# Kernel optimization log

Measured on AMD Instinct MI355X. Metric: run time of the kernel, lower is better.

Reference implementation:

```python
import jax, jax.numpy as jnp
import numpy as np

N_NODES = 100000
N_EDGES = 1600000
N_GRAPHS = 1000
F_IN, HID = 9, 64


def _glorot(key, shape):
    fan_in, fan_out = shape[0], shape[1]
    lim = (6.0 / (fan_in + fan_out)) ** 0.5
    return jax.random.uniform(key, shape, jnp.float32, -lim, lim)


def setup_inputs() -> dict:
    key = jax.random.key(0)
    ks = jax.random.split(key, 12)
    x = jax.random.normal(ks[0], (N_NODES, F_IN), jnp.float32)
    edge_index = jax.random.randint(ks[1], (2, N_EDGES), 0, N_NODES, jnp.int64)
    edge_attr = jnp.zeros((N_EDGES, 1), jnp.float32)
    batch = jnp.sort(jax.random.randint(ks[2], (N_NODES,), 0, N_GRAPHS, jnp.int64))
    # SAGEConv layer 1: 9 -> 64 (lin_l on aggregated neighbors w/ bias, lin_r on root)
    Wl1 = _glorot(ks[3], (F_IN, HID)); Wr1 = _glorot(ks[4], (F_IN, HID)); b1 = jnp.zeros((HID,), jnp.float32)
    # SAGEConv layer 2: 64 -> 64
    Wl2 = _glorot(ks[5], (HID, HID)); Wr2 = _glorot(ks[6], (HID, HID)); b2 = jnp.zeros((HID,), jnp.float32)
    # MLP readout: 64 -> 32 -> 1
    Wm1 = _glorot(ks[7], (HID, HID // 2)); bm1 = jnp.zeros((HID // 2,), jnp.float32)
    Wm2 = _glorot(ks[8], (HID // 2, 1)); bm2 = jnp.zeros((1,), jnp.float32)
    return dict(x=x, edge_index=edge_index, edge_attr=edge_attr, batch=batch,
                Wl1=Wl1, Wr1=Wr1, b1=b1, Wl2=Wl2, Wr2=Wr2, b2=b2,
                Wm1=Wm1, bm1=bm1, Wm2=Wm2, bm2=bm2)


def _sage_conv(x, src, dst, Wl, Wr, b, n_nodes):
    # mean aggregation of source-node features onto target nodes
    msgs = x[src]                                              # [E, F] gather
    s = jax.ops.segment_sum(msgs, dst, num_segments=n_nodes)   # [N, F] scatter-add
    cnt = jax.ops.segment_sum(jnp.ones((src.shape[0],), x.dtype), dst, num_segments=n_nodes)
    agg = s / jnp.maximum(cnt, 1.0)[:, None]
    return agg @ Wl + x @ Wr + b


def reference(x, edge_index, edge_attr, batch,
              Wl1, Wr1, b1, Wl2, Wr2, b2, Wm1, bm1, Wm2, bm2):
    src, dst = edge_index[0], edge_index[1]
    n = x.shape[0]
    h = jax.nn.relu(_sage_conv(x, src, dst, Wl1, Wr1, b1, n))
    h = _sage_conv(h, src, dst, Wl2, Wr2, b2, n)               # no act after last layer
    # global mean pool over graphs
    gs = jax.ops.segment_sum(h, batch, num_segments=N_GRAPHS)
    gc = jax.ops.segment_sum(jnp.ones((n,), h.dtype), batch, num_segments=N_GRAPHS)
    xg = gs / jnp.maximum(gc, 1.0)[:, None]                    # [G, 64]
    out = jax.nn.sigmoid(jax.nn.relu(xg @ Wm1 + bm1) @ Wm2 + bm2)  # [G, 1]
    return out
```

## Files before the change

kernel.cpp:

```cpp
#include <hip/hip_runtime.h>
#include <math.h>

#define N_NODES  100000
#define N_EDGES  1600000
#define N_GRAPHS 1000
#define F_IN     9
#define HID      64
#define NBUCK    196
#define BCAP     12288
#define CHUNK    4096
#define NZERO    128200
#define NPB      32

typedef unsigned int uint32;
typedef unsigned short ushort16;
typedef float v2f __attribute__((ext_vector_type(2)));


__device__ __forceinline__ uint32 pk_lo(float a, float b, uint32 old) {
    return (uint32)__builtin_amdgcn_cvt_pk_fp8_f32(a, b, (int)old, false);
}
__device__ __forceinline__ uint32 pk_hi(float a, float b, uint32 old) {
    return (uint32)__builtin_amdgcn_cvt_pk_fp8_f32(a, b, (int)old, true);
}
__device__ __forceinline__ float bfl(uint32 w) { return __uint_as_float(w << 16); }
__device__ __forceinline__ float bfh(uint32 w) { return __uint_as_float(w & 0xffff0000u); }
__device__ __forceinline__ uint32 f2bf1(float f) {
    uint32 u = __float_as_uint(f);
    u += 0x7fffu + ((u >> 16) & 1u);
    return u >> 16;
}
__device__ __forceinline__ uint32 bfpair(float lo, float hi) {
    return f2bf1(lo) | (f2bf1(hi) << 16);
}

__global__ __launch_bounds__(256) void zero_kernel(float4* __restrict__ ws) {
    int i = blockIdx.x * 256 + threadIdx.x;
    if (i * 4 < NZERO)
        ws[i] = make_float4(0.f, 0.f, 0.f, 0.f);
}

__global__ __launch_bounds__(256) void pad_part_kernel(const float* __restrict__ x,
                                                       const int* __restrict__ ei,
                                                       int* __restrict__ gcur,
                                                       int* __restrict__ ebuf,
                                                       uint32* __restrict__ x8b) {
    __shared__ int lcnt[NBUCK], lbase[NBUCK];
    int tid = threadIdx.x;

    int n = blockIdx.x * 256 + tid;
    if (n < N_NODES) {
        uint32 w[4];
        #pragma unroll
        for (int p = 0; p < 4; ++p) {
            float v0 = (4 * p + 0 < F_IN) ? x[(size_t)n * F_IN + 4 * p + 0] : 0.0f;
            float v1 = (4 * p + 1 < F_IN) ? x[(size_t)n * F_IN + 4 * p + 1] : 0.0f;
            float v2 = (4 * p + 2 < F_IN) ? x[(size_t)n * F_IN + 4 * p + 2] : 0.0f;
            float v3 = (4 * p + 3 < F_IN) ? x[(size_t)n * F_IN + 4 * p + 3] : 0.0f;
            w[p] = pk_hi(v2, v3, pk_lo(v0, v1, 0u));
        }
        *reinterpret_cast<uint4*>(&x8b[(size_t)n * 4]) =
            make_uint4(w[0], w[1], w[2], w[3]);
    }

    for (int i = tid; i < NBUCK; i += 256) lcnt[i] = 0;
    __syncthreads();
    int e0 = blockIdx.x * CHUNK;
    int e1 = e0 + CHUNK; if (e1 > N_EDGES) e1 = N_EDGES;
    for (int e = e0 + tid; e < e1; e += 256)
        atomicAdd(&lcnt[ei[N_EDGES + e] >> 9], 1);
    __syncthreads();
    for (int i = tid; i < NBUCK; i += 256)
        lbase[i] = atomicAdd(&gcur[i], lcnt[i]);
    __syncthreads();
    for (int i = tid; i < NBUCK; i += 256) lcnt[i] = 0;
    __syncthreads();
    for (int e = e0 + tid; e < e1; e += 256) {
        int src = ei[e];
        int dst = ei[N_EDGES + e];
        int b = dst >> 9;
        int pos = lbase[b] + atomicAdd(&lcnt[b], 1);
        if (pos < BCAP)
            ebuf[(size_t)b * BCAP + pos] = src | ((dst & 511) << 17);
    }
}

__global__ __launch_bounds__(512) void build_csr_kernel(const int* __restrict__ ebuf,
                                                        const int* __restrict__ gcur,
                                                        int2* __restrict__ rowcnt,
                                                        int* __restrict__ col) {
    __shared__ int cnt[512];
    __shared__ int cur[512];
    __shared__ int wsum[8];
    int b = blockIdx.x;
    int n0 = b << 9;
    int tid = threadIdx.x;
    int ec = gcur[b]; if (ec > BCAP) ec = BCAP;
    size_t base = (size_t)b * BCAP;
    cnt[tid] = 0;
    __syncthreads();
    for (int e = tid; e < ec; e += 512)
        atomicAdd(&cnt[(uint32)ebuf[base + e] >> 17], 1);
    __syncthreads();
    int v = cnt[tid];
    int lane = tid & 63, wid = tid >> 6;
    int s = v;
    #pragma unroll
    for (int off = 1; off < 64; off <<= 1) {
        int u = __shfl_up(s, off, 64);
        if (lane >= off) s += u;
    }
    if (lane == 63) wsum[wid] = s;
    __syncthreads();
    int add = 0;
    for (int w = 0; w < wid; ++w) add += wsum[w];
    int off_ex = s - v + add;
    int n = n0 + tid;
    if (n < N_NODES) rowcnt[n] = make_int2((int)base + off_ex, v);
    cur[tid] = off_ex;
    __syncthreads();
    for (int e = tid; e < ec; e += 512) {
        int pv = ebuf[base + e];
        int pos = atomicAdd(&cur[(uint32)pv >> 17], 1);
        col[base + pos] = pv & 0x1FFFF;
    }
}

__global__ __launch_bounds__(256) void agg_l1_kernel(const float* __restrict__ x,
                                                     const uint32* __restrict__ x8b,
                                                     const int2* __restrict__ rowcnt,
                                                     const int* __restrict__ col,
                                                     const float* __restrict__ Wl1,
                                                     const float* __restrict__ Wr1,
                                                     const float* __restrict__ b1,
                                                     const int* __restrict__ batch,
                                                     uint32* __restrict__ h1b,
                                                     float* __restrict__ poolH) {
    __shared__ float  w1s[F_IN * 128];
    __shared__ float  bs[HID];
    __shared__ float  ss[NPB * 20];
    __shared__ float  xs[NPB * 10];
    __shared__ uint32 hsp[NPB * 33];
    int tid = threadIdx.x;
    int n0 = blockIdx.x * NPB;
    for (int i = tid; i < F_IN * HID; i += 256) {
        int f = i >> 6, j = i & 63;
        w1s[f * 128 + j]      = Wl1[i];
        w1s[f * 128 + 64 + j] = Wr1[i];
    }
    if (tid < HID) bs[tid] = b1[tid];
    for (int i = tid; i < NPB * F_IN; i += 256) {
        int r = i / F_IN, f = i - r * F_IN;
        xs[r * 10 + f] = x[(size_t)(n0 + r) * F_IN + f];
    }

    {
        int r = tid >> 3, s = (tid >> 2) & 1, q = tid & 3;
        int2 rc = rowcnt[n0 + r];
        int deg = rc.y;
        v2f a01 = {0.f, 0.f}, a23 = {0.f, 0.f};
        int i = s;
        for (; i + 6 < deg; i += 8) {
            int c0 = col[rc.x + i];
            int c1 = col[rc.x + i + 2];
            int c2 = col[rc.x + i + 4];
            int c3 = col[rc.x + i + 6];
            uint32 d0 = x8b[(size_t)c0 * 4 + q];
            uint32 d1 = x8b[(size_t)c1 * 4 + q];
            uint32 d2 = x8b[(size_t)c2 * 4 + q];
            uint32 d3 = x8b[(size_t)c3 * 4 + q];
            a01 += __builtin_amdgcn_cvt_pk_f32_fp8((int)d0, false);
            a23 += __builtin_amdgcn_cvt_pk_f32_fp8((int)d0, true);
            a01 += __builtin_amdgcn_cvt_pk_f32_fp8((int)d1, false);
            a23 += __builtin_amdgcn_cvt_pk_f32_fp8((int)d1, true);
            a01 += __builtin_amdgcn_cvt_pk_f32_fp8((int)d2, false);
            a23 += __builtin_amdgcn_cvt_pk_f32_fp8((int)d2, true);
            a01 += __builtin_amdgcn_cvt_pk_f32_fp8((int)d3, false);
            a23 += __builtin_amdgcn_cvt_pk_f32_fp8((int)d3, true);
        }
        for (; i < deg; i += 2) {
            uint32 d0 = x8b[(size_t)col[rc.x + i] * 4 + q];
            a01 += __builtin_amdgcn_cvt_pk_f32_fp8((int)d0, false);
            a23 += __builtin_amdgcn_cvt_pk_f32_fp8((int)d0, true);
        }
        float r4[4] = {a01[0], a01[1], a23[0], a23[1]};
        #pragma unroll
        for (int k = 0; k < 4; ++k)
            r4[k] += __shfl_xor(r4[k], 4, 64);
        if (s == 0) {
            float inv = 1.0f / fmaxf((float)deg, 1.0f);
            *reinterpret_cast<float4*>(&ss[r * 20 + q * 4]) =
                make_float4(r4[0] * inv, r4[1] * inv, r4[2] * inv, r4[3] * inv);
        }
    }
    __syncthreads();

    int r = tid >> 3, cg = tid & 7, k0 = cg * 8;
    float h[8];
    #pragma unroll
    for (int kk = 0; kk < 8; ++kk) {
        int k = k0 + kk;
        float v = bs[k];
        #pragma unroll
        for (int f = 0; f < F_IN; ++f)
            v += ss[r * 20 + f] * w1s[f * 128 + k]
               + xs[r * 10 + f] * w1s[f * 128 + 64 + k];
        h[kk] = fmaxf(v, 0.0f);
    }
    int n = n0 + r;
    {
        uint32 w0 = pk_hi(h[2], h[3], pk_lo(h[0], h[1], 0u));
        uint32 w1 = pk_hi(h[6], h[7], pk_lo(h[4], h[5], 0u));
        *reinterpret_cast<uint2*>(&h1b[(size_t)n * 16 + cg * 2]) =
            make_uint2(w0, w1);
    }
    {
        hsp[r * 33 + cg * 4 + 0] = bfpair(h[0], h[1]);
        hsp[r * 33 + cg * 4 + 1] = bfpair(h[2], h[3]);
        hsp[r * 33 + cg * 4 + 2] = bfpair(h[4], h[5]);
        hsp[r * 33 + cg * 4 + 3] = bfpair(h[6], h[7]);
    }
    __syncthreads();
    if (tid < HID) {
        int j = tid;
        int wsel = j >> 1;
        bool hi = (j & 1) != 0;
        int cur = batch[n0];
        uint32 w0 = hsp[wsel];
        float v = hi ? bfh(w0) : bfl(w0);
        for (int rr = 1; rr < NPB; ++rr) {
            int g = batch[n0 + rr];
            uint32 wr = hsp[rr * 33 + wsel];
            float val = hi ? bfh(wr) : bfl(wr);
            if (g == cur) v += val;
            else { atomicAdd(&poolH[cur * HID + j], v); cur = g; v = val; }
        }
        atomicAdd(&poolH[cur * HID + j], v);
    }
}

__global__ __launch_bounds__(256) void gather2_kernel(const uint32* __restrict__ h1b,
                                                      const int2* __restrict__ rowcnt,
                                                      const int* __restrict__ col,
                                                      const int* __restrict__ batch,
                                                      float* __restrict__ poolA) {
    __shared__ float sh[4][HID];
    int w = threadIdx.x >> 6;
    int lane = threadIdx.x & 63;
    int slot = lane >> 3;
    int grp  = lane & 7;
    int n = blockIdx.x * 4 + w;
    int2 rc = rowcnt[n];
    const uint32* hb = h1b + grp * 2;
    v2f a0 = {0.f, 0.f}, a1 = {0.f, 0.f}, a2 = {0.f, 0.f}, a3 = {0.f, 0.f};
    int i = rc.x + slot;
    int end = rc.x + rc.y;
    for (; i + 8 < end; i += 16) {
        int c0 = col[i];
        int c1 = col[i + 8];
        uint2 d0 = *reinterpret_cast<const uint2*>(hb + (size_t)c0 * 16);
        uint2 d1 = *reinterpret_cast<const uint2*>(hb + (size_t)c1 * 16);
        a0 += __builtin_amdgcn_cvt_pk_f32_fp8((int)d0.x, false);
        a1 += __builtin_amdgcn_cvt_pk_f32_fp8((int)d0.x, true);
        a2 += __builtin_amdgcn_cvt_pk_f32_fp8((int)d0.y, false);
        a3 += __builtin_amdgcn_cvt_pk_f32_fp8((int)d0.y, true);
        a0 += __builtin_amdgcn_cvt_pk_f32_fp8((int)d1.x, false);
        a1 += __builtin_amdgcn_cvt_pk_f32_fp8((int)d1.x, true);
        a2 += __builtin_amdgcn_cvt_pk_f32_fp8((int)d1.y, false);
        a3 += __builtin_amdgcn_cvt_pk_f32_fp8((int)d1.y, true);
    }
    if (i < end) {
        int c0 = col[i];
        uint2 d0 = *reinterpret_cast<const uint2*>(hb + (size_t)c0 * 16);
        a0 += __builtin_amdgcn_cvt_pk_f32_fp8((int)d0.x, false);
        a1 += __builtin_amdgcn_cvt_pk_f32_fp8((int)d0.x, true);
        a2 += __builtin_amdgcn_cvt_pk_f32_fp8((int)d0.y, false);
        a3 += __builtin_amdgcn_cvt_pk_f32_fp8((int)d0.y, true);
    }
    float r8[8] = {a0[0], a0[1], a1[0], a1[1], a2[0], a2[1], a3[0], a3[1]};
    #pragma unroll
    for (int k = 0; k < 8; ++k) {
        r8[k] += __shfl_xor(r8[k], 8, 64);
        r8[k] += __shfl_xor(r8[k], 16, 64);
        r8[k] += __shfl_xor(r8[k], 32, 64);
    }
    float inv = 1.0f / fmaxf((float)rc.y, 1.0f);
    if (slot == 0) {
        #pragma unroll
        for (int k = 0; k < 8; ++k)
            sh[w][grp * 8 + k] = r8[k] * inv;
    }
    __syncthreads();
    if (threadIdx.x < HID) {
        int j = threadIdx.x;
        int base = blockIdx.x * 4;
        int cur = batch[base];
        float v = sh[0][j];
        #pragma unroll
        for (int r = 1; r < 4; ++r) {
            int g = batch[base + r];
            float val = sh[r][j];
            if (g == cur) v += val;
            else { atomicAdd(&poolA[cur * HID + j], v); cur = g; v = val; }
        }
        atomicAdd(&poolA[cur * HID + j], v);
    }
}

__global__ void mlp_kernel(const float* __restrict__ poolA,
                           const float* __restrict__ poolH,
                           const int* __restrict__ batch,
                           const float* __restrict__ Wl2,
                           const float* __restrict__ Wr2,
                           const float* __restrict__ b2,
                           const float* __restrict__ Wm1,
                           const float* __restrict__ bm1,
                           const float* __restrict__ Wm2,
                           const float* __restrict__ bm2,
                           float* __restrict__ out) {
    __shared__ float spA[4][HID], spH[4][HID], sx[4][HID];
    int t = blockIdx.x * blockDim.x + threadIdx.x;
    int g = t >> 6;
    int j = t & 63;
    int w = threadIdx.x >> 6;
    if (g >= N_GRAPHS) return;
    int lo = 0, hi = N_NODES;
    while (lo < hi) { int m = (lo + hi) >> 1; if (batch[m] < g) lo = m + 1; else hi = m; }
    int start = lo;
    lo = 0; hi = N_NODES;
    while (lo < hi) { int m = (lo + hi) >> 1; if (batch[m] < g + 1) lo = m + 1; else hi = m; }
    int cntg = lo - start;
    float inv = 1.0f / fmaxf((float)cntg, 1.0f);
    spA[w][j] = poolA[g * HID + j];
    spH[w][j] = poolH[g * HID + j];
    float acc = 0.0f;
    #pragma unroll 8
    for (int k = 0; k < HID; ++k)
        acc += spA[w][k] * Wl2[k * HID + j] + spH[w][k] * Wr2[k * HID + j];
    sx[w][j] = acc * inv + b2[j];
    if (j < 32) {
        float a = bm1[j];
        #pragma unroll 8
        for (int k = 0; k < HID; ++k)
            a += sx[w][k] * Wm1[k * 32 + j];
        float r = fmaxf(a, 0.0f) * Wm2[j];
        #pragma unroll
        for (int off = 16; off > 0; off >>= 1)
            r += __shfl_down(r, off, 32);
        if (j == 0)
            out[g] = 1.0f / (1.0f + expf(-(r + bm2[0])));
    }
}

extern "C" void kernel_launch(void* const* d_in, const int* in_sizes, int n_in,
                              void* d_out, int out_size, void* d_ws, size_t ws_size,
                              hipStream_t stream) {
    const float* x    = (const float*)d_in[0];
    const int*   ei   = (const int*)d_in[1];
    const int*   batch= (const int*)d_in[3];
    const float* Wl1  = (const float*)d_in[4];
    const float* Wr1  = (const float*)d_in[5];
    const float* b1   = (const float*)d_in[6];
    const float* Wl2  = (const float*)d_in[7];
    const float* Wr2  = (const float*)d_in[8];
    const float* b2   = (const float*)d_in[9];
    const float* Wm1  = (const float*)d_in[10];
    const float* bm1  = (const float*)d_in[11];
    const float* Wm2  = (const float*)d_in[12];
    const float* bm2  = (const float*)d_in[13];
    float* out = (float*)d_out;

    int*   wsi = (int*)d_ws;
    float* wsf = (float*)d_ws;
    float*  poolA  = wsf;
    float*  poolH  = wsf + 64000;
    int*    gcur   = wsi + 128000;
    int2*   rowcnt = (int2*)(wsi + 128200);
    int*    col    = wsi + 328200;
    int*    ebuf   = wsi + 2736648;
    uint32* x8b    = (uint32*)(wsi + 5145096);
    uint32* h1b    = (uint32*)(wsi + 5545096);

    {   int bl = (NZERO / 4 + 255) / 256;
        zero_kernel<<<bl, 256, 0, stream>>>((float4*)d_ws);
    }
    {   int bl = (N_EDGES + CHUNK - 1) / CHUNK;
        pad_part_kernel<<<bl, 256, 0, stream>>>(x, ei, gcur, ebuf, x8b);
    }
    build_csr_kernel<<<NBUCK, 512, 0, stream>>>(ebuf, gcur, rowcnt, col);
    {   int th = 256, bl = N_NODES / NPB;
        agg_l1_kernel<<<bl, th, 0, stream>>>(x, x8b, rowcnt, col, Wl1, Wr1, b1,
                                             batch, h1b, poolH);
    }
    {   int th = 256, bl = N_NODES / 4;
        gather2_kernel<<<bl, th, 0, stream>>>(h1b, rowcnt, col, batch, poolA);
    }
    {   int th = 256, bl = (N_GRAPHS * 64) / th;
        mlp_kernel<<<bl, th, 0, stream>>>(poolA, poolH, batch,
                                          Wl2, Wr2, b2, Wm1, bm1, Wm2, bm2, out);
    }
}
```

Baseline: 130.2 us.

## Process two nodes per wave in gather2 and widen CSR build blocks

gather2 now has each wavefront aggregate two destination nodes in an interleaved loop, which doubles the independent gather loads in flight and halves the block count and pool atomics per node. build_csr uses 1024-thread blocks so more threads share the edge counting and scatter passes, while the scan stays on the first 512 threads. The cost is more register pressure and some divergence in the tail loops when the two nodes have different degrees.

```diff
diff --git a/kernel.cpp b/kernel.cpp
--- a/kernel.cpp
+++ b/kernel.cpp
@@ -13,7 +13,6 @@
 #define NPB      32
 
 typedef unsigned int uint32;
-typedef unsigned short ushort16;
 typedef float v2f __attribute__((ext_vector_type(2)));
 
 
@@ -32,6 +31,28 @@
 }
 __device__ __forceinline__ uint32 bfpair(float lo, float hi) {
     return f2bf1(lo) | (f2bf1(hi) << 16);
+}
+
+__device__ __forceinline__ void acc2(const uint32* __restrict__ hb, int c0, int c1,
+                                     v2f& a0, v2f& a1, v2f& a2, v2f& a3) {
+    uint2 d0 = *reinterpret_cast<const uint2*>(hb + (size_t)c0 * 16);
+    uint2 d1 = *reinterpret_cast<const uint2*>(hb + (size_t)c1 * 16);
+    a0 += __builtin_amdgcn_cvt_pk_f32_fp8((int)d0.x, false);
+    a1 += __builtin_amdgcn_cvt_pk_f32_fp8((int)d0.x, true);
+    a2 += __builtin_amdgcn_cvt_pk_f32_fp8((int)d0.y, false);
+    a3 += __builtin_amdgcn_cvt_pk_f32_fp8((int)d0.y, true);
+    a0 += __builtin_amdgcn_cvt_pk_f32_fp8((int)d1.x, false);
+    a1 += __builtin_amdgcn_cvt_pk_f32_fp8((int)d1.x, true);
+    a2 += __builtin_amdgcn_cvt_pk_f32_fp8((int)d1.y, false);
+    a3 += __builtin_amdgcn_cvt_pk_f32_fp8((int)d1.y, true);
+}
+__device__ __forceinline__ void acc1(const uint32* __restrict__ hb, int c0,
+                                     v2f& a0, v2f& a1, v2f& a2, v2f& a3) {
+    uint2 d0 = *reinterpret_cast<const uint2*>(hb + (size_t)c0 * 16);
+    a0 += __builtin_amdgcn_cvt_pk_f32_fp8((int)d0.x, false);
+    a1 += __builtin_amdgcn_cvt_pk_f32_fp8((int)d0.x, true);
+    a2 += __builtin_amdgcn_cvt_pk_f32_fp8((int)d0.y, false);
+    a3 += __builtin_amdgcn_cvt_pk_f32_fp8((int)d0.y, true);
 }
 
 __global__ __launch_bounds__(256) void zero_kernel(float4* __restrict__ ws) {
@@ -85,10 +106,10 @@
     }
 }
 
-__global__ __launch_bounds__(512) void build_csr_kernel(const int* __restrict__ ebuf,
-                                                        const int* __restrict__ gcur,
-                                                        int2* __restrict__ rowcnt,
-                                                        int* __restrict__ col) {
+__global__ __launch_bounds__(1024) void build_csr_kernel(const int* __restrict__ ebuf,
+                                                         const int* __restrict__ gcur,
+                                                         int2* __restrict__ rowcnt,
+                                                         int* __restrict__ col) {
     __shared__ int cnt[512];
     __shared__ int cur[512];
     __shared__ int wsum[8];
@@ -97,29 +118,34 @@
     int tid = threadIdx.x;
     int ec = gcur[b]; if (ec > BCAP) ec = BCAP;
     size_t base = (size_t)b * BCAP;
-    cnt[tid] = 0;
-    __syncthreads();
-    for (int e = tid; e < ec; e += 512)
+    if (tid < 512) cnt[tid] = 0;
+    __syncthreads();
+    for (int e = tid; e < ec; e += 1024)
         atomicAdd(&cnt[(uint32)ebuf[base + e] >> 17], 1);
     __syncthreads();
-    int v = cnt[tid];
+    int v = 0, s = 0;
     int lane = tid & 63, wid = tid >> 6;
-    int s = v;
-    #pragma unroll
-    for (int off = 1; off < 64; off <<= 1) {
-        int u = __shfl_up(s, off, 64);
-        if (lane >= off) s += u;
-    }
-    if (lane == 63) wsum[wid] = s;
-    __syncthreads();
-    int add = 0;
-    for (int w = 0; w < wid; ++w) add += wsum[w];
-    int off_ex = s - v + add;
-    int n = n0 + tid;
-    if (n < N_NODES) rowcnt[n] = make_int2((int)base + off_ex, v);
-    cur[tid] = off_ex;
-    __syncthreads();
-    for (int e = tid; e < ec; e += 512) {
+    if (tid < 512) {
+        v = cnt[tid];
+        s = v;
+        #pragma unroll
+        for (int off = 1; off < 64; off <<= 1) {
+            int u = __shfl_up(s, off, 64);
+            if (lane >= off) s += u;
+        }
+        if (lane == 63) wsum[wid] = s;
+    }
+    __syncthreads();
+    if (tid < 512) {
+        int add = 0;
+        for (int w = 0; w < wid; ++w) add += wsum[w];
+        int off_ex = s - v + add;
+        int n = n0 + tid;
+        if (n < N_NODES) rowcnt[n] = make_int2((int)base + off_ex, v);
+        cur[tid] = off_ex;
+    }
+    __syncthreads();
+    for (int e = tid; e < ec; e += 1024) {
         int pv = ebuf[base + e];
         int pos = atomicAdd(&cur[(uint32)pv >> 17], 1);
         col[base + pos] = pv & 0x1FFFF;
@@ -244,60 +270,66 @@
                                                       const int* __restrict__ col,
                                                       const int* __restrict__ batch,
                                                       float* __restrict__ poolA) {
-    __shared__ float sh[4][HID];
+    __shared__ float sh[8][HID];
     int w = threadIdx.x >> 6;
     int lane = threadIdx.x & 63;
     int slot = lane >> 3;
     int grp  = lane & 7;
-    int n = blockIdx.x * 4 + w;
-    int2 rc = rowcnt[n];
+    int base = blockIdx.x * 8;
+    int nA = base + w * 2;
+    int nB = nA + 1;
+    int2 rcA = rowcnt[nA];
+    int2 rcB = rowcnt[nB];
     const uint32* hb = h1b + grp * 2;
-    v2f a0 = {0.f, 0.f}, a1 = {0.f, 0.f}, a2 = {0.f, 0.f}, a3 = {0.f, 0.f};
-    int i = rc.x + slot;
-    int end = rc.x + rc.y;
-    for (; i + 8 < end; i += 16) {
-        int c0 = col[i];
-        int c1 = col[i + 8];
-        uint2 d0 = *reinterpret_cast<const uint2*>(hb + (size_t)c0 * 16);
-        uint2 d1 = *reinterpret_cast<const uint2*>(hb + (size_t)c1 * 16);
-        a0 += __builtin_amdgcn_cvt_pk_f32_fp8((int)d0.x, false);
-        a1 += __builtin_amdgcn_cvt_pk_f32_fp8((int)d0.x, true);
-        a2 += __builtin_amdgcn_cvt_pk_f32_fp8((int)d0.y, false);
-        a3 += __builtin_amdgcn_cvt_pk_f32_fp8((int)d0.y, true);
-        a0 += __builtin_amdgcn_cvt_pk_f32_fp8((int)d1.x, false);
-        a1 += __builtin_amdgcn_cvt_pk_f32_fp8((int)d1.x, true);
-        a2 += __builtin_amdgcn_cvt_pk_f32_fp8((int)d1.y, false);
-        a3 += __builtin_amdgcn_cvt_pk_f32_fp8((int)d1.y, true);
-    }
-    if (i < end) {
-        int c0 = col[i];
-        uint2 d0 = *reinterpret_cast<const uint2*>(hb + (size_t)c0 * 16);
-        a0 += __builtin_amdgcn_cvt_pk_f32_fp8((int)d0.x, false);
-        a1 += __builtin_amdgcn_cvt_pk_f32_fp8((int)d0.x, true);
-        a2 += __builtin_amdgcn_cvt_pk_f32_fp8((int)d0.y, false);
-        a3 += __builtin_amdgcn_cvt_pk_f32_fp8((int)d0.y, true);
-    }
-    float r8[8] = {a0[0], a0[1], a1[0], a1[1], a2[0], a2[1], a3[0], a3[1]};
+    v2f aA0 = {0.f,0.f}, aA1 = {0.f,0.f}, aA2 = {0.f,0.f}, aA3 = {0.f,0.f};
+    v2f aB0 = {0.f,0.f}, aB1 = {0.f,0.f}, aB2 = {0.f,0.f}, aB3 = {0.f,0.f};
+    int iA = rcA.x + slot, endA = rcA.x + rcA.y;
+    int iB = rcB.x + slot, endB = rcB.x + rcB.y;
+    while (iA + 8 < endA && iB + 8 < endB) {
+        int cA0 = col[iA], cA1 = col[iA + 8];
+        int cB0 = col[iB], cB1 = col[iB + 8];
+        acc2(hb, cA0, cA1, aA0, aA1, aA2, aA3);
+        acc2(hb, cB0, cB1, aB0, aB1, aB2, aB3);
+        iA += 16; iB += 16;
+    }
+    for (; iA + 8 < endA; iA += 16) {
+        int c0 = col[iA], c1 = col[iA + 8];
+        acc2(hb, c0, c1, aA0, aA1, aA2, aA3);
+    }
+    if (iA < endA) acc1(hb, col[iA], aA0, aA1, aA2, aA3);
+    for (; iB + 8 < endB; iB += 16) {
+        int c0 = col[iB], c1 = col[iB + 8];
+        acc2(hb, c0, c1, aB0, aB1, aB2, aB3);
+    }
+    if (iB < endB) acc1(hb, col[iB], aB0, aB1, aB2, aB3);
+
+    float rA[8] = {aA0[0], aA0[1], aA1[0], aA1[1], aA2[0], aA2[1], aA3[0], aA3[1]};
+    float rB[8] = {aB0[0], aB0[1], aB1[0], aB1[1], aB2[0], aB2[1], aB3[0], aB3[1]};
+    float invA = 1.0f / fmaxf((float)rcA.y, 1.0f);
+    float invB = 1.0f / fmaxf((float)rcB.y, 1.0f);
     #pragma unroll
     for (int k = 0; k < 8; ++k) {
-        r8[k] += __shfl_xor(r8[k], 8, 64);
-        r8[k] += __shfl_xor(r8[k], 16, 64);
-        r8[k] += __shfl_xor(r8[k], 32, 64);
-    }
-    float inv = 1.0f / fmaxf((float)rc.y, 1.0f);
+        rA[k] += __shfl_xor(rA[k], 8, 64);
+        rA[k] += __shfl_xor(rA[k], 16, 64);
+        rA[k] += __shfl_xor(rA[k], 32, 64);
+        rB[k] += __shfl_xor(rB[k], 8, 64);
+        rB[k] += __shfl_xor(rB[k], 16, 64);
+        rB[k] += __shfl_xor(rB[k], 32, 64);
+    }
     if (slot == 0) {
         #pragma unroll
-        for (int k = 0; k < 8; ++k)
-            sh[w][grp * 8 + k] = r8[k] * inv;
+        for (int k = 0; k < 8; ++k) {
+            sh[w * 2 + 0][grp * 8 + k] = rA[k] * invA;
+            sh[w * 2 + 1][grp * 8 + k] = rB[k] * invB;
+        }
     }
     __syncthreads();
     if (threadIdx.x < HID) {
         int j = threadIdx.x;
-        int base = blockIdx.x * 4;
         int cur = batch[base];
         float v = sh[0][j];
         #pragma unroll
-        for (int r = 1; r < 4; ++r) {
+        for (int r = 1; r < 8; ++r) {
             int g = batch[base + r];
             float val = sh[r][j];
             if (g == cur) v += val;
@@ -387,12 +419,12 @@
     {   int bl = (N_EDGES + CHUNK - 1) / CHUNK;
         pad_part_kernel<<<bl, 256, 0, stream>>>(x, ei, gcur, ebuf, x8b);
     }
-    build_csr_kernel<<<NBUCK, 512, 0, stream>>>(ebuf, gcur, rowcnt, col);
+    build_csr_kernel<<<NBUCK, 1024, 0, stream>>>(ebuf, gcur, rowcnt, col);
     {   int th = 256, bl = N_NODES / NPB;
         agg_l1_kernel<<<bl, th, 0, stream>>>(x, x8b, rowcnt, col, Wl1, Wr1, b1,
                                              batch, h1b, poolH);
     }
-    {   int th = 256, bl = N_NODES / 4;
+    {   int th = 256, bl = N_NODES / 8;
         gather2_kernel<<<bl, th, 0, stream>>>(h1b, rowcnt, col, batch, poolA);
     }
     {   int th = 256, bl = (N_GRAPHS * 64) / th;
```

Result: faster. 125.5 us, median of 2 (-3.6%).
